# Optimization experiments

Measured on AMD Instinct MI355X. Metric: run time of the kernel, lower is better.

The kernel has to match this reference:

```python
import jax, jax.numpy as jnp
import numpy as np

N_NODES = 50000
N_EDGES = 800000
OBS_DIM = 25
HID = 128
EMB = 64
EDGE_DIM = 8
HEADS = 4
N_LAYERS = 3
COMM_RANGE = 1500.0
LN_EPS = 1e-5


def layernorm(x, g, b):
    mu = jnp.mean(x, axis=-1, keepdims=True)
    var = jnp.mean((x - mu) ** 2, axis=-1, keepdims=True)
    return (x - mu) / jnp.sqrt(var + LN_EPS) * g + b


def setup_inputs() -> dict:
    key = jax.random.key(0)
    ks = iter(jax.random.split(key, 64))

    def w(shape, s=0.05):
        return (jax.random.normal(next(ks), shape, jnp.float32) * s).astype(jnp.float32)

    inp = {}
    inp["observations"] = jax.random.normal(next(ks), (N_NODES, OBS_DIM), jnp.float32)
    inp["positions"] = jax.random.uniform(next(ks), (N_NODES, 2), jnp.float32) * 1000.0
    inp["edge_index"] = jax.random.randint(next(ks), (2, N_EDGES), 0, N_NODES, jnp.int32)
    # node encoder (obs_encoder branch: Linear-LN-ReLU-Linear-ReLU)
    inp["enc_w1"] = w((OBS_DIM, HID)); inp["enc_b1"] = w((HID,), 0.01)
    inp["enc_ln_g"] = jnp.ones((HID,), jnp.float32); inp["enc_ln_b"] = jnp.zeros((HID,), jnp.float32)
    inp["enc_w2"] = w((HID, EMB)); inp["enc_b2"] = w((EMB,), 0.01)
    cat_dim = 2 * EMB + EDGE_DIM  # 136
    # per-layer GNN params, stacked over layers
    inp["msg_w1"] = w((N_LAYERS, cat_dim, HID)); inp["msg_b1"] = w((N_LAYERS, HID), 0.01)
    inp["msg_w2"] = w((N_LAYERS, HID, EMB)); inp["msg_b2"] = w((N_LAYERS, EMB), 0.01)
    inp["att_w1"] = w((N_LAYERS, cat_dim, HID)); inp["att_b1"] = w((N_LAYERS, HID), 0.01)
    inp["att_w2"] = w((N_LAYERS, HID, HEADS)); inp["att_b2"] = w((N_LAYERS, HEADS), 0.01)
    inp["upd_w1"] = w((N_LAYERS, 2 * EMB, HID)); inp["upd_b1"] = w((N_LAYERS, HID), 0.01)
    inp["upd_w2"] = w((N_LAYERS, HID, EMB)); inp["upd_b2"] = w((N_LAYERS, EMB), 0.01)
    inp["ln_g"] = jnp.ones((N_LAYERS, EMB), jnp.float32); inp["ln_b"] = jnp.zeros((N_LAYERS, EMB), jnp.float32)
    # output projection
    inp["out_w1"] = w((EMB, HID)); inp["out_b1"] = w((HID,), 0.01)
    inp["out_w2"] = w((HID, EMB)); inp["out_b2"] = w((EMB,), 0.01)
    return inp


def reference(observations, positions, edge_index,
              enc_w1, enc_b1, enc_ln_g, enc_ln_b, enc_w2, enc_b2,
              msg_w1, msg_b1, msg_w2, msg_b2,
              att_w1, att_b1, att_w2, att_b2,
              upd_w1, upd_b1, upd_w2, upd_b2,
              ln_g, ln_b,
              out_w1, out_b1, out_w2, out_b2):
    n = observations.shape[0]
    # --- node encoder (use_full_obs=True path) ---
    h = observations @ enc_w1 + enc_b1
    h = jax.nn.relu(layernorm(h, enc_ln_g, enc_ln_b))
    x = jax.nn.relu(h @ enc_w2 + enc_b2)  # [N, EMB]

    # --- edge features (build_graph math, edges given) ---
    src, dst = edge_index[0], edge_index[1]
    rel = positions[dst] - positions[src]                    # [E, 2]
    dist = jnp.linalg.norm(rel, axis=-1, keepdims=True)      # [E, 1]
    rel_n = rel / (dist + 1e-6)
    dist_n = dist / COMM_RANGE
    angle = jnp.arctan2(rel[:, 1], rel[:, 0])[:, None]
    edge_attr = jnp.concatenate(
        [dist_n, rel_n, jnp.cos(angle), jnp.sin(angle), dist_n ** 2,
         jnp.zeros((rel.shape[0], 2), x.dtype)], axis=-1)    # [E, 8]

    # --- GNN communication layers (PyG: x_i = target = dst, x_j = source = src,
    #     aggregate to dst; dropout inactive at inference) ---
    for l in range(N_LAYERS):
        cat = jnp.concatenate([x[dst], x[src], edge_attr], axis=-1)       # [E, 136]
        m = jax.nn.relu(cat @ msg_w1[l] + msg_b1[l]) @ msg_w2[l] + msg_b2[l]   # [E, EMB]
        a = jax.nn.relu(cat @ att_w1[l] + att_b1[l]) @ att_w2[l] + att_b2[l]   # [E, HEADS]
        wgt = jnp.mean(jax.nn.softmax(a, axis=-1), axis=-1, keepdims=True)     # [E, 1]
        aggr = jax.ops.segment_sum(m * wgt, dst, num_segments=n)               # [N, EMB]
        upd_in = jnp.concatenate([x, aggr], axis=-1)                            # [N, 2*EMB]
        upd = jax.nn.relu(upd_in @ upd_w1[l] + upd_b1[l]) @ upd_w2[l] + upd_b2[l]
        x = layernorm(x + upd, ln_g[l], ln_b[l])

    # --- output projection ---
    return jax.nn.relu(x @ out_w1 + out_b1) @ out_w2 + out_b2
```

## Files before the change

### kernel.cpp

```cpp
#include <hip/hip_runtime.h>
#include <hip/hip_bf16.h>

typedef unsigned short ushort_t;
typedef unsigned int uint_t;

constexpr int OBS  = 25;
constexpr int HID  = 128;
constexpr int EMB  = 64;
constexpr int CAT  = 136;
constexpr int NN   = 50000;

constexpr int TE      = 128;
constexpr int ETHR    = 256;
constexpr int K1PAD   = 148;
constexpr int K2PAD   = 140;
constexpr int K1STEPS = 9;
constexpr int K2STEPS = 8;

constexpr int TB = 128;

typedef __attribute__((ext_vector_type(8)))  short bf16x8;
typedef __attribute__((ext_vector_type(16))) float f32x16;
typedef __attribute__((ext_vector_type(4)))  uint_t uint4v;

__device__ __forceinline__ ushort_t f2bf(float f) {
    union { float f; uint_t u; } v; v.f = f;
    uint_t r = v.u + 0x7FFFu + ((v.u >> 16) & 1u);
    return (ushort_t)(r >> 16);
}

__device__ __forceinline__ bf16x8 ld8(const ushort_t* p) {
    uint2 lo = *reinterpret_cast<const uint2*>(p);
    uint2 hi = *reinterpret_cast<const uint2*>(p + 4);
    uint4 u = make_uint4(lo.x, lo.y, hi.x, hi.y);
    return __builtin_bit_cast(bf16x8, u);
}

#define CROW(R, LHI) (4 * (LHI) + ((R) & 3) + 8 * ((R) >> 2))

__global__ __launch_bounds__(256) void k_hist(
    const int* __restrict__ dst, int* __restrict__ hist, int ne)
{
    int e = blockIdx.x * 256 + threadIdx.x;
    if (e < ne) atomicAdd(&hist[dst[e]], 1);
}

__global__ __launch_bounds__(512) void k_scan1(
    const int* __restrict__ hist, int* __restrict__ scanned,
    int* __restrict__ bsum, int nk)
{
    __shared__ int s[512];
    int t = threadIdx.x, i = blockIdx.x * 512 + t;
    int v = (i < nk) ? hist[i] : 0;
    s[t] = v; __syncthreads();
#pragma unroll
    for (int off = 1; off < 512; off <<= 1) {
        int x = (t >= off) ? s[t - off] : 0;
        __syncthreads();
        s[t] += x;
        __syncthreads();
    }
    if (i < nk) scanned[i] = s[t] - v;
    if (t == 511) bsum[blockIdx.x] = s[511];
}

__global__ __launch_bounds__(512) void k_scan3(
    int* __restrict__ scanned, const int* __restrict__ bsum, int nk)
{
    __shared__ int pref;
    if (threadIdx.x == 0) {
        int run = 0;
        for (int b = 0; b < (int)blockIdx.x; ++b) run += bsum[b];
        pref = run;
    }
    __syncthreads();
    int i = blockIdx.x * 512 + threadIdx.x;
    if (i < nk) scanned[i] += pref;
}

__global__ __launch_bounds__(256) void k_scatter_feat(
    const float* __restrict__ pos, const int* __restrict__ src,
    const int* __restrict__ dst, int* __restrict__ ofs,
    uint4v* __restrict__ eab4, int ne)
{
    int e = blockIdx.x * 256 + threadIdx.x;
    if (e >= ne) return;
    int s = src[e], d = dst[e];
    float rx = pos[d * 2 + 0] - pos[s * 2 + 0];
    float ry = pos[d * 2 + 1] - pos[s * 2 + 1];
    float dist = sqrtf(rx * rx + ry * ry);
    float inv = 1.f / (dist + 1e-6f);
    float dn = dist * (1.f / 1500.f);
    uint_t ux = (uint_t)f2bf(dn) | ((uint_t)f2bf(rx * inv) << 16);
    uint_t uy = (uint_t)f2bf(ry * inv) | ((dist > 0.f ? 0u : 1u) << 16);
    int p = atomicAdd(&ofs[d], 1);
    uint4v ev = { ux, uy, (uint_t)s, (uint_t)d };
    eab4[p] = ev;
}

__global__ __launch_bounds__(256) void k_prep(
    const float* __restrict__ w1, const float* __restrict__ w2,
    ushort_t* __restrict__ w1t, ushort_t* __restrict__ w2t)
{
    int t = blockIdx.x * 256 + threadIdx.x;
    const int n1 = 3 * HID * K1PAD;
    if (t < n1) {
        int l = t / (HID * K1PAD), rem = t % (HID * K1PAD);
        int c = rem / K1PAD, k = rem % K1PAD;
        float v = (k < CAT) ? w1[(size_t)l * CAT * HID + (size_t)k * HID + c] : 0.f;
        w1t[t] = f2bf(v);
    }
    const int n2 = 3 * EMB * K2PAD;
    if (t < n2) {
        int l = t / (EMB * K2PAD), rem = t % (EMB * K2PAD);
        int c = rem / K2PAD, k = rem % K2PAD;
        float v = (k < HID) ? w2[(size_t)l * HID * EMB + (size_t)k * EMB + c] : 0.f;
        w2t[t] = f2bf(v);
    }
}

constexpr int EKP = 36;
__global__ __launch_bounds__(256, 1) void k_encoder_mfma(
    const float* __restrict__ obs,
    const float* __restrict__ w1, const float* __restrict__ b1,
    const float* __restrict__ lng, const float* __restrict__ lnb,
    const float* __restrict__ w2, const float* __restrict__ b2,
    float* __restrict__ x, ushort_t* __restrict__ xb, int n)
{
    __shared__ __align__(16) ushort_t s_OB[TB * EKP];
    __shared__ __align__(16) ushort_t s_B1[HID * EKP];
    __shared__ __align__(16) float    s_G[TB * 132];
    __shared__ __align__(16) ushort_t s_H[TB * K2PAD];
    __shared__ __align__(16) ushort_t s_W2[EMB * K2PAD];

    const int tid = threadIdx.x;
    const int lane = tid & 63, wid = tid >> 6;
    const int wr = wid >> 1, wc = wid & 1;
    const int l31 = lane & 31, lhi = lane >> 5;
    const int n0 = blockIdx.x * TB;

    for (int i = tid; i < TB * 32; i += 256) {
        int row = i >> 5, k = i & 31;
        int gn = n0 + row;
        float v = (gn < n && k < OBS) ? obs[(size_t)gn * OBS + k] : 0.f;
        s_OB[row * EKP + k] = f2bf(v);
    }
    for (int i = tid; i < 32 * HID; i += 256) {
        int k = i >> 7, c = i & 127;
        float v = (k < OBS) ? w1[k * HID + c] : 0.f;
        s_B1[c * EKP + k] = f2bf(v);
    }
    __syncthreads();

    f32x16 a00, a01, a10, a11;
    {
        float bv0 = b1[wc * 64 + l31], bv1 = b1[wc * 64 + 32 + l31];
#pragma unroll
        for (int i = 0; i < 16; ++i) { a00[i] = bv0; a01[i] = bv1; a10[i] = bv0; a11[i] = bv1; }
    }
    {
        const ushort_t* aR0 = s_OB + (wr * 64 + l31) * EKP;
        const ushort_t* aR1 = aR0 + 32 * EKP;
        const ushort_t* bR0 = s_B1 + (wc * 64 + l31) * EKP;
        const ushort_t* bR1 = bR0 + 32 * EKP;
        const int koff = lhi * 8;
#pragma unroll
        for (int s = 0; s < 2; ++s) {
            const int ke = s * 16 + koff;
            bf16x8 av0 = ld8(aR0 + ke), av1 = ld8(aR1 + ke);
            bf16x8 bv0 = ld8(bR0 + ke), bv1 = ld8(bR1 + ke);
            a00 = __builtin_amdgcn_mfma_f32_32x32x16_bf16(av0, bv0, a00, 0, 0, 0);
            a01 = __builtin_amdgcn_mfma_f32_32x32x16_bf16(av0, bv1, a01, 0, 0, 0);
            a10 = __builtin_amdgcn_mfma_f32_32x32x16_bf16(av1, bv0, a10, 0, 0, 0);
            a11 = __builtin_amdgcn_mfma_f32_32x32x16_bf16(av1, bv1, a11, 0, 0, 0);
        }
    }
#define WRITE_G(ACC, SUB, NC)                                                  \
    {                                                                          \
        const int col = wc * 64 + (NC) * 32 + l31;                             \
        _Pragma("unroll")                                                      \
        for (int r = 0; r < 16; ++r) {                                         \
            int row = wr * 64 + (SUB) * 32 + CROW(r, lhi);                     \
            s_G[row * 132 + col] = ACC[r];                                     \
        }                                                                      \
    }
    WRITE_G(a00, 0, 0) WRITE_G(a01, 0, 1) WRITE_G(a10, 1, 0) WRITE_G(a11, 1, 1)
#undef WRITE_G
    __syncthreads();

    for (int i = tid; i < HID * EMB; i += 256) {
        int k = i >> 6, c = i & 63;
        s_W2[c * K2PAD + k] = f2bf(w2[i]);
    }
    if (tid < TB) {
        float sum = 0.f, sum2 = 0.f;
        const float* gr = s_G + tid * 132;
#pragma unroll 8
        for (int q = 0; q < HID; ++q) { float v = gr[q]; sum += v; sum2 += v * v; }
        float mu = sum * (1.f / HID);
        float var = fmaxf(sum2 * (1.f / HID) - mu * mu, 0.f);
        float rs = 1.f / sqrtf(var + 1e-5f);
        ushort_t* hr = s_H + tid * K2PAD;
#pragma unroll 8
        for (int q = 0; q < HID; ++q) {
            float v = (gr[q] - mu) * rs * lng[q] + lnb[q];
            hr[q] = f2bf(fmaxf(v, 0.f));
        }
    }
    __syncthreads();

    f32x16 c0, c1;
    {
        float bv = b2[wc * 32 + l31];
#pragma unroll
        for (int i = 0; i < 16; ++i) { c0[i] = bv; c1[i] = bv; }
    }
    {
        const ushort_t* aR0 = s_H + (wr * 64 + l31) * K2PAD;
        const ushort_t* aR1 = aR0 + 32 * K2PAD;
        const ushort_t* bR = s_W2 + (wc * 32 + l31) * K2PAD;
        const int koff = lhi * 8;
#pragma unroll
        for (int s = 0; s < K2STEPS; ++s) {
            const int ke = s * 16 + koff;
            bf16x8 av0 = ld8(aR0 + ke), av1 = ld8(aR1 + ke);
            bf16x8 bv = ld8(bR + ke);
            c0 = __builtin_amdgcn_mfma_f32_32x32x16_bf16(av0, bv, c0, 0, 0, 0);
            c1 = __builtin_amdgcn_mfma_f32_32x32x16_bf16(av1, bv, c1, 0, 0, 0);
        }
    }
    {
        const int col = wc * 32 + l31;
#define STORE_X(CC, SUB)                                                       \
        {                                                                      \
            _Pragma("unroll")                                                  \
            for (int r = 0; r < 16; ++r) {                                     \
                int row = wr * 64 + (SUB) * 32 + CROW(r, lhi);                 \
                int gn = n0 + row;                                             \
                if (gn < n) {                                                  \
                    float v = fmaxf(CC[r], 0.f);                               \
                    x[(size_t)gn * EMB + col] = v;                             \
                    xb[(size_t)gn * EMB + col] = f2bf(v);                      \
                }                                                              \
            }                                                                  \
        }
        STORE_X(c0, 0) STORE_X(c1, 1)
#undef STORE_X
    }
}

__global__ __launch_bounds__(ETHR, 4) void k_edge_mfma(
    const ushort_t* __restrict__ xb,
    const uint4v* __restrict__ eab4,
    const ushort_t* __restrict__ w1t,
    const float* __restrict__ b1,
    const ushort_t* __restrict__ w2t,
    const float* __restrict__ b2,
    float* __restrict__ aggr, int ne)
{
    __shared__ __align__(16) ushort_t s_A[TE * K1PAD];
    __shared__ int s_dst[TE];
    ushort_t* s_H = s_A;
    float*    s_M = reinterpret_cast<float*>(s_A);

    const int tid  = threadIdx.x;
    const int lane = tid & 63, wid = tid >> 6;
    const int wr = wid >> 1, wc = wid & 1;
    const int l31 = lane & 31, lhi = lane >> 5;
    const int e0 = blockIdx.x * TE;

    {
        const int e = tid >> 1, h = tid & 1, ge = e0 + e;
        ushort_t* arow = s_A + e * K1PAD;
        uint4v ev = eab4[ge];
        if (h == 0) {
            s_dst[e] = (int)ev.w;
            const uint2* sp = reinterpret_cast<const uint2*>(xb + (size_t)ev.w * EMB);
            uint2* dp = reinterpret_cast<uint2*>(arow);
#pragma unroll
            for (int i = 0; i < 16; ++i) dp[i] = sp[i];
        } else {
            const uint2* sp = reinterpret_cast<const uint2*>(xb + (size_t)ev.z * EMB);
            uint2* dp = reinterpret_cast<uint2*>(arow + EMB);
#pragma unroll
            for (int i = 0; i < 16; ++i) dp[i] = sp[i];
            uint_t dn_b = ev.x & 0xFFFFu, rxn_b = ev.x >> 16;
            uint_t ryn_b = ev.y & 0xFFFFu, flag = ev.y >> 16;
            uint_t cos_b = flag ? 0x3F80u : rxn_b;
            uint_t sin_b = flag ? 0u : ryn_b;
            union { uint_t u; float f; } cv; cv.u = dn_b << 16;
            uint_t dn2_b = (uint_t)f2bf(cv.f * cv.f);
            uint2* ap = reinterpret_cast<uint2*>(arow + 2 * EMB);
            ap[0] = make_uint2(dn_b | (rxn_b << 16), ryn_b | (cos_b << 16));
            ap[1] = make_uint2(sin_b | (dn2_b << 16), 0u);
            uint2* pp = reinterpret_cast<uint2*>(arow + CAT);
            pp[0] = make_uint2(0u, 0u); pp[1] = make_uint2(0u, 0u);
            pp[2] = make_uint2(0u, 0u);
        }
    }
    __syncthreads();

    f32x16 a00, a01, a10, a11;
    {
        float bv0 = b1[wc * 64 + l31], bv1 = b1[wc * 64 + 32 + l31];
#pragma unroll
        for (int i = 0; i < 16; ++i) { a00[i] = bv0; a01[i] = bv1; a10[i] = bv0; a11[i] = bv1; }
    }
    {
        const ushort_t* aR0 = s_A + (wr * 64 + l31) * K1PAD;
        const ushort_t* aR1 = aR0 + 32 * K1PAD;
        const ushort_t* bR0 = w1t + (wc * 64 + l31) * K1PAD;
        const ushort_t* bR1 = bR0 + 32 * K1PAD;
        const int koff = lhi * 8;
#pragma unroll
        for (int s = 0; s < K1STEPS; ++s) {
            const int ke = s * 16 + koff;
            bf16x8 av0 = ld8(aR0 + ke);
            bf16x8 av1 = ld8(aR1 + ke);
            bf16x8 bv0 = ld8(bR0 + ke);
            bf16x8 bv1 = ld8(bR1 + ke);
            a00 = __builtin_amdgcn_mfma_f32_32x32x16_bf16(av0, bv0, a00, 0, 0, 0);
            a01 = __builtin_amdgcn_mfma_f32_32x32x16_bf16(av0, bv1, a01, 0, 0, 0);
            a10 = __builtin_amdgcn_mfma_f32_32x32x16_bf16(av1, bv0, a10, 0, 0, 0);
            a11 = __builtin_amdgcn_mfma_f32_32x32x16_bf16(av1, bv1, a11, 0, 0, 0);
        }
    }
    __syncthreads();

#define WRITE_H(ACC, SUB, NC)                                                  \
    {                                                                          \
        const int col = wc * 64 + (NC) * 32 + l31;                             \
        _Pragma("unroll")                                                      \
        for (int r = 0; r < 16; ++r) {                                         \
            int row = wr * 64 + (SUB) * 32 + CROW(r, lhi);                     \
            s_H[row * K2PAD + col] = f2bf(fmaxf(ACC[r], 0.f));                 \
        }                                                                      \
    }
    WRITE_H(a00, 0, 0) WRITE_H(a01, 0, 1) WRITE_H(a10, 1, 0) WRITE_H(a11, 1, 1)
#undef WRITE_H
    __syncthreads();

    f32x16 c0, c1;
    {
        float bv = b2[wc * 32 + l31];
#pragma unroll
        for (int i = 0; i < 16; ++i) { c0[i] = bv; c1[i] = bv; }
    }
    {
        const ushort_t* aR0 = s_H + (wr * 64 + l31) * K2PAD;
        const ushort_t* aR1 = aR0 + 32 * K2PAD;
        const ushort_t* bR = w2t + (wc * 32 + l31) * K2PAD;
        const int koff = lhi * 8;
#pragma unroll
        for (int s = 0; s < K2STEPS; ++s) {
            const int ke = s * 16 + koff;
            bf16x8 av0 = ld8(aR0 + ke);
            bf16x8 av1 = ld8(aR1 + ke);
            bf16x8 bv = ld8(bR + ke);
            c0 = __builtin_amdgcn_mfma_f32_32x32x16_bf16(av0, bv, c0, 0, 0, 0);
            c1 = __builtin_amdgcn_mfma_f32_32x32x16_bf16(av1, bv, c1, 0, 0, 0);
        }
    }
    __syncthreads();

    {
        const int col = wc * 32 + l31;
#pragma unroll
        for (int r = 0; r < 16; ++r) {
            int row = wr * 64 + CROW(r, lhi);
            s_M[row * 68 + col] = c0[r] * 0.25f;
            s_M[(row + 32) * 68 + col] = c1[r] * 0.25f;
        }
    }
    __syncthreads();

    {
        const int col = tid & 63, g = tid >> 6, base = g * 32;
        int cur = s_dst[base];
        float acc = 0.f;
#pragma unroll 8
        for (int r = 0; r < 32; ++r) {
            int d = s_dst[base + r];
            float v = s_M[(base + r) * 68 + col];
            if (d != cur) {
                atomicAdd(aggr + (size_t)cur * EMB + col, acc);
                acc = 0.f; cur = d;
            }
            acc += v;
        }
        atomicAdd(aggr + (size_t)cur * EMB + col, acc);
    }
}

__global__ __launch_bounds__(256, 2) void k_update_mfma(
    float* __restrict__ x, ushort_t* __restrict__ xb,
    float* __restrict__ aggr,
    const float* __restrict__ w1, const float* __restrict__ b1,
    const float* __restrict__ w2, const float* __restrict__ b2,
    const float* __restrict__ g, const float* __restrict__ bb, int n)
{
    __shared__ __align__(16) ushort_t s_A[TB * K2PAD];
    __shared__ __align__(16) ushort_t s_B[TB * K2PAD];
    ushort_t* s_H  = s_A;
    ushort_t* s_W2 = s_B;
    float*    s_U  = reinterpret_cast<float*>(s_B);

    const int tid = threadIdx.x;
    const int lane = tid & 63, wid = tid >> 6;
    const int wr = wid >> 1, wc = wid & 1;
    const int l31 = lane & 31, lhi = lane >> 5;
    const int n0 = blockIdx.x * TB;

    {
        const int row = tid >> 1, h = tid & 1;
        const int gn = n0 + row;
        ushort_t* arow = s_A + row * K2PAD;
        if (h == 0) {
            uint2* dp = reinterpret_cast<uint2*>(arow);
            if (gn < n) {
                const uint2* sp = reinterpret_cast<const uint2*>(xb + (size_t)gn * EMB);
#pragma unroll
                for (int i = 0; i < 16; ++i) dp[i] = sp[i];
            } else {
                const uint2 z = make_uint2(0u, 0u);
#pragma unroll
                for (int i = 0; i < 16; ++i) dp[i] = z;
            }
        } else {
            if (gn < n) {
                float4* sp = reinterpret_cast<float4*>(aggr + (size_t)gn * EMB);
                const float4 z4 = make_float4(0.f, 0.f, 0.f, 0.f);
#pragma unroll
                for (int i = 0; i < 16; ++i) {
                    float4 v = sp[i];
                    sp[i] = z4;
                    ushort_t* qq = arow + EMB + i * 4;
                    qq[0] = f2bf(v.x); qq[1] = f2bf(v.y); qq[2] = f2bf(v.z); qq[3] = f2bf(v.w);
                }
            } else {
#pragma unroll
                for (int i = 0; i < 16; ++i) {
                    ushort_t* qq = arow + EMB + i * 4;
                    qq[0] = 0; qq[1] = 0; qq[2] = 0; qq[3] = 0;
                }
            }
        }
    }
    for (int i = tid; i < 128 * 128; i += 256) {
        int k = i >> 7, c = i & 127;
        s_B[c * K2PAD + k] = f2bf(w1[i]);
    }
    __syncthreads();

    f32x16 a00, a01, a10, a11;
    {
        float bv0 = b1[wc * 64 + l31], bv1 = b1[wc * 64 + 32 + l31];
#pragma unroll
        for (int i = 0; i < 16; ++i) { a00[i] = bv0; a01[i] = bv1; a10[i] = bv0; a11[i] = bv1; }
    }
    {
        const ushort_t* aR0 = s_A + (wr * 64 + l31) * K2PAD;
        const ushort_t* aR1 = aR0 + 32 * K2PAD;
        const ushort_t* bR0 = s_B + (wc * 64 + l31) * K2PAD;
        const ushort_t* bR1 = bR0 + 32 * K2PAD;
        const int koff = lhi * 8;
#pragma unroll
        for (int s = 0; s < K2STEPS; ++s) {
            const int ke = s * 16 + koff;
            bf16x8 av0 = ld8(aR0 + ke), av1 = ld8(aR1 + ke);
            bf16x8 bv0 = ld8(bR0 + ke), bv1 = ld8(bR1 + ke);
            a00 = __builtin_amdgcn_mfma_f32_32x32x16_bf16(av0, bv0, a00, 0, 0, 0);
            a01 = __builtin_amdgcn_mfma_f32_32x32x16_bf16(av0, bv1, a01, 0, 0, 0);
            a10 = __builtin_amdgcn_mfma_f32_32x32x16_bf16(av1, bv0, a10, 0, 0, 0);
            a11 = __builtin_amdgcn_mfma_f32_32x32x16_bf16(av1, bv1, a11, 0, 0, 0);
        }
    }
    __syncthreads();

#define WRITE_H(ACC, SUB, NC)                                                  \
    {                                                                          \
        const int col = wc * 64 + (NC) * 32 + l31;                             \
        _Pragma("unroll")                                                      \
        for (int r = 0; r < 16; ++r) {                                         \
            int row = wr * 64 + (SUB) * 32 + CROW(r, lhi);                     \
            s_H[row * K2PAD + col] = f2bf(fmaxf(ACC[r], 0.f));                 \
        }                                                                      \
    }
    WRITE_H(a00, 0, 0) WRITE_H(a01, 0, 1) WRITE_H(a10, 1, 0) WRITE_H(a11, 1, 1)
#undef WRITE_H
    for (int i = tid; i < HID * EMB; i += 256) {
        int k = i >> 6, c = i & 63;
        s_W2[c * K2PAD + k] = f2bf(w2[i]);
    }
    __syncthreads();

    f32x16 c0, c1;
    {
        float bv = b2[wc * 32 + l31];
#pragma unroll
        for (int i = 0; i < 16; ++i) { c0[i] = bv; c1[i] = bv; }
    }
    {
        const ushort_t* aR0 = s_H + (wr * 64 + l31) * K2PAD;
        const ushort_t* aR1 = aR0 + 32 * K2PAD;
        const ushort_t* bR = s_W2 + (wc * 32 + l31) * K2PAD;
        const int koff = lhi * 8;
#pragma unroll
        for (int s = 0; s < K2STEPS; ++s) {
            const int ke = s * 16 + koff;
            bf16x8 av0 = ld8(aR0 + ke), av1 = ld8(aR1 + ke);
            bf16x8 bv = ld8(bR + ke);
            c0 = __builtin_amdgcn_mfma_f32_32x32x16_bf16(av0, bv, c0, 0, 0, 0);
            c1 = __builtin_amdgcn_mfma_f32_32x32x16_bf16(av1, bv, c1, 0, 0, 0);
        }
    }
    __syncthreads();

    {
        const int col = wc * 32 + l31;
#pragma unroll
        for (int r = 0; r < 16; ++r) {
            int row = wr * 64 + CROW(r, lhi);
            s_U[row * 68 + col] = c0[r];
            s_U[(row + 32) * 68 + col] = c1[r];
        }
    }
    __syncthreads();

    if (tid < TB) {
        int gn = n0 + tid;
        if (gn < n) {
            const float* xr = x + (size_t)gn * EMB;
            float* ur = s_U + tid * 68;
            float sum = 0.f, sum2 = 0.f;
#pragma unroll 8
            for (int q = 0; q < EMB; ++q) {
                float v = xr[q] + ur[q];
                ur[q] = v;
                sum += v; sum2 += v * v;
            }
            float mu = sum * (1.f / EMB);
            float var = fmaxf(sum2 * (1.f / EMB) - mu * mu, 0.f);
            float rs = 1.f / sqrtf(var + 1e-5f);
            float* xo = x + (size_t)gn * EMB;
            ushort_t* xbo = xb + (size_t)gn * EMB;
#pragma unroll 8
            for (int q = 0; q < EMB; ++q) {
                float v = (ur[q] - mu) * rs * g[q] + bb[q];
                xo[q] = v;
                xbo[q] = f2bf(v);
            }
        }
    }
}

constexpr int OKP = 68;
__global__ __launch_bounds__(256, 2) void k_output_mfma(
    const ushort_t* __restrict__ xb,
    const float* __restrict__ w1, const float* __restrict__ b1,
    const float* __restrict__ w2, const float* __restrict__ b2,
    float* __restrict__ out, int n)
{
    __shared__ __align__(16) ushort_t s_A[TB * OKP];
    __shared__ __align__(16) ushort_t s_B[HID * OKP];
    __shared__ __align__(16) ushort_t s_H[TB * K2PAD];
    __shared__ __align__(16) ushort_t s_W2[EMB * K2PAD];

    const int tid = threadIdx.x;
    const int lane = tid & 63, wid = tid >> 6;
    const int wr = wid >> 1, wc = wid & 1;
    const int l31 = lane & 31, lhi = lane >> 5;
    const int n0 = blockIdx.x * TB;

    for (int i = tid; i < TB * 16; i += 256) {
        int row = i >> 4, q = i & 15;
        int gn = n0 + row;
        uint2 v = make_uint2(0u, 0u);
        if (gn < n) v = reinterpret_cast<const uint2*>(xb + (size_t)gn * EMB)[q];
        *reinterpret_cast<uint2*>(s_A + row * OKP + q * 4) = v;
    }
    for (int i = tid; i < EMB * HID; i += 256) {
        int k = i >> 7, c = i & 127;
        s_B[c * OKP + k] = f2bf(w1[i]);
    }
    for (int i = tid; i < HID * EMB; i += 256) {
        int k = i >> 6, c = i & 63;
        s_W2[c * K2PAD + k] = f2bf(w2[i]);
    }
    __syncthreads();

    f32x16 a00, a01, a10, a11;
    {
        float bv0 = b1[wc * 64 + l31], bv1 = b1[wc * 64 + 32 + l31];
#pragma unroll
        for (int i = 0; i < 16; ++i) { a00[i] = bv0; a01[i] = bv1; a10[i] = bv0; a11[i] = bv1; }
    }
    {
        const ushort_t* aR0 = s_A + (wr * 64 + l31) * OKP;
        const ushort_t* aR1 = aR0 + 32 * OKP;
        const ushort_t* bR0 = s_B + (wc * 64 + l31) * OKP;
        const ushort_t* bR1 = bR0 + 32 * OKP;
        const int koff = lhi * 8;
#pragma unroll
        for (int s = 0; s < 4; ++s) {
            const int ke = s * 16 + koff;
            bf16x8 av0 = ld8(aR0 + ke), av1 = ld8(aR1 + ke);
            bf16x8 bv0 = ld8(bR0 + ke), bv1 = ld8(bR1 + ke);
            a00 = __builtin_amdgcn_mfma_f32_32x32x16_bf16(av0, bv0, a00, 0, 0, 0);
            a01 = __builtin_amdgcn_mfma_f32_32x32x16_bf16(av0, bv1, a01, 0, 0, 0);
            a10 = __builtin_amdgcn_mfma_f32_32x32x16_bf16(av1, bv0, a10, 0, 0, 0);
            a11 = __builtin_amdgcn_mfma_f32_32x32x16_bf16(av1, bv1, a11, 0, 0, 0);
        }
    }
    __syncthreads();

#define WRITE_H(ACC, SUB, NC)                                                  \
    {                                                                          \
        const int col = wc * 64 + (NC) * 32 + l31;                             \
        _Pragma("unroll")                                                      \
        for (int r = 0; r < 16; ++r) {                                         \
            int row = wr * 64 + (SUB) * 32 + CROW(r, lhi);                     \
            s_H[row * K2PAD + col] = f2bf(fmaxf(ACC[r], 0.f));                 \
        }                                                                      \
    }
    WRITE_H(a00, 0, 0) WRITE_H(a01, 0, 1) WRITE_H(a10, 1, 0) WRITE_H(a11, 1, 1)
#undef WRITE_H
    __syncthreads();

    f32x16 c0, c1;
    {
        float bv = b2[wc * 32 + l31];
#pragma unroll
        for (int i = 0; i < 16; ++i) { c0[i] = bv; c1[i] = bv; }
    }
    {
        const ushort_t* aR0 = s_H + (wr * 64 + l31) * K2PAD;
        const ushort_t* aR1 = aR0 + 32 * K2PAD;
        const ushort_t* bR = s_W2 + (wc * 32 + l31) * K2PAD;
        const int koff = lhi * 8;
#pragma unroll
        for (int s = 0; s < K2STEPS; ++s) {
            const int ke = s * 16 + koff;
            bf16x8 av0 = ld8(aR0 + ke), av1 = ld8(aR1 + ke);
            bf16x8 bv = ld8(bR + ke);
            c0 = __builtin_amdgcn_mfma_f32_32x32x16_bf16(av0, bv, c0, 0, 0, 0);
            c1 = __builtin_amdgcn_mfma_f32_32x32x16_bf16(av1, bv, c1, 0, 0, 0);
        }
    }
    {
        const int col = wc * 32 + l31;
#pragma unroll
        for (int r = 0; r < 16; ++r) {
            int row0 = wr * 64 + CROW(r, lhi);
            int g0 = n0 + row0, g1 = g0 + 32;
            if (g0 < n) out[(size_t)g0 * EMB + col] = c0[r];
            if (g1 < n) out[(size_t)g1 * EMB + col] = c1[r];
        }
    }
}

extern "C" void kernel_launch(void* const* d_in, const int* in_sizes, int n_in,
                              void* d_out, int out_size, void* d_ws, size_t ws_size,
                              hipStream_t stream)
{
    const float* obs     = (const float*)d_in[0];
    const float* pos     = (const float*)d_in[1];
    const int*   eidx    = (const int*)d_in[2];
    const float* enc_w1  = (const float*)d_in[3];
    const float* enc_b1  = (const float*)d_in[4];
    const float* enc_lng = (const float*)d_in[5];
    const float* enc_lnb = (const float*)d_in[6];
    const float* enc_w2  = (const float*)d_in[7];
    const float* enc_b2  = (const float*)d_in[8];
    const float* msg_w1  = (const float*)d_in[9];
    const float* msg_b1  = (const float*)d_in[10];
    const float* msg_w2  = (const float*)d_in[11];
    const float* msg_b2  = (const float*)d_in[12];
    const float* upd_w1  = (const float*)d_in[17];
    const float* upd_b1  = (const float*)d_in[18];
    const float* upd_w2  = (const float*)d_in[19];
    const float* upd_b2  = (const float*)d_in[20];
    const float* ln_g    = (const float*)d_in[21];
    const float* ln_b    = (const float*)d_in[22];
    const float* out_w1  = (const float*)d_in[23];
    const float* out_b1  = (const float*)d_in[24];
    const float* out_w2  = (const float*)d_in[25];
    const float* out_b2  = (const float*)d_in[26];

    const int n  = in_sizes[0] / OBS;
    const int ne = in_sizes[2] / 2;
    const int* src = eidx;
    const int* dst = eidx + ne;

    char* ws = (char*)d_ws;
    float*    x     = (float*)ws;
    ushort_t* xbuf  = (ushort_t*)(ws + 12800000);
    uint4v*   eab4  = (uint4v*)(ws + 19200000);
    float*    aggr  = (float*)(ws + 32000000);
    ushort_t* w1t   = (ushort_t*)(ws + 44800000);
    ushort_t* w2t   = (ushort_t*)(ws + 44913664);
    int*      hist  = (int*)(ws + 44967424);
    int*      scan  = (int*)(ws + 45167424);
    int*      bsum  = (int*)(ws + 45367424);

    const int NB1 = (NN + 511) / 512;
    const int nb  = (n + TB - 1) / TB;

    hipMemsetAsync(hist, 0, NN * sizeof(int), stream);
    k_hist<<<(ne + 255) / 256, 256, 0, stream>>>(dst, hist, ne);
    k_scan1<<<NB1, 512, 0, stream>>>(hist, scan, bsum, NN);
    k_scan3<<<NB1, 512, 0, stream>>>(scan, bsum, NN);
    k_scatter_feat<<<(ne + 255) / 256, 256, 0, stream>>>(pos, src, dst, scan,
                                                         eab4, ne);

    k_prep<<<(3 * HID * K1PAD + 255) / 256, 256, 0, stream>>>(msg_w1, msg_w2, w1t, w2t);
    k_encoder_mfma<<<nb, 256, 0, stream>>>(obs, enc_w1, enc_b1, enc_lng, enc_lnb,
                                           enc_w2, enc_b2, x, xbuf, n);
    hipMemsetAsync(aggr, 0, (size_t)n * EMB * sizeof(float), stream);

    for (int l = 0; l < 3; ++l) {
        k_edge_mfma<<<ne / TE, ETHR, 0, stream>>>(
            xbuf, eab4,
            w1t + (size_t)l * HID * K1PAD, msg_b1 + (size_t)l * HID,
            w2t + (size_t)l * EMB * K2PAD, msg_b2 + (size_t)l * EMB,
            aggr, ne);
        k_update_mfma<<<nb, 256, 0, stream>>>(
            x, xbuf, aggr,
            upd_w1 + (size_t)l * 2 * EMB * HID, upd_b1 + (size_t)l * HID,
            upd_w2 + (size_t)l * HID * EMB, upd_b2 + (size_t)l * EMB,
            ln_g + (size_t)l * EMB, ln_b + (size_t)l * EMB, n);
    }
    k_output_mfma<<<nb, 256, 0, stream>>>(
        xbuf, out_w1, out_b1, out_w2, out_b2, (float*)d_out, n);
}
```

Measured before the change: 754.9 us.

## Double edge-kernel threads to 512 and split MFMA tiles across eight waves

```diff
diff --git a/kernel.cpp b/kernel.cpp
--- a/kernel.cpp
+++ b/kernel.cpp
@@ -11,7 +11,7 @@
 constexpr int NN   = 50000;
 
 constexpr int TE      = 128;
-constexpr int ETHR    = 256;
+constexpr int ETHR    = 512;
 constexpr int K1PAD   = 148;
 constexpr int K2PAD   = 140;
 constexpr int K1STEPS = 9;
@@ -249,7 +249,7 @@
     }
 }
 
-__global__ __launch_bounds__(ETHR, 4) void k_edge_mfma(
+__global__ __launch_bounds__(ETHR, 8) void k_edge_mfma(
     const ushort_t* __restrict__ xb,
     const uint4v* __restrict__ eab4,
     const ushort_t* __restrict__ w1t,
@@ -270,7 +270,7 @@
     const int e0 = blockIdx.x * TE;
 
     {
-        const int e = tid >> 1, h = tid & 1, ge = e0 + e;
+        const int e = tid >> 2, h = tid & 3, ge = e0 + e;
         ushort_t* arow = s_A + e * K1PAD;
         uint4v ev = eab4[ge];
         if (h == 0) {
@@ -278,12 +278,22 @@
             const uint2* sp = reinterpret_cast<const uint2*>(xb + (size_t)ev.w * EMB);
             uint2* dp = reinterpret_cast<uint2*>(arow);
 #pragma unroll
-            for (int i = 0; i < 16; ++i) dp[i] = sp[i];
-        } else {
+            for (int i = 0; i < 8; ++i) dp[i] = sp[i];
+        } else if (h == 1) {
+            const uint2* sp = reinterpret_cast<const uint2*>(xb + (size_t)ev.w * EMB) + 8;
+            uint2* dp = reinterpret_cast<uint2*>(arow) + 8;
+#pragma unroll
+            for (int i = 0; i < 8; ++i) dp[i] = sp[i];
+        } else if (h == 2) {
             const uint2* sp = reinterpret_cast<const uint2*>(xb + (size_t)ev.z * EMB);
             uint2* dp = reinterpret_cast<uint2*>(arow + EMB);
 #pragma unroll
-            for (int i = 0; i < 16; ++i) dp[i] = sp[i];
+            for (int i = 0; i < 8; ++i) dp[i] = sp[i];
+        } else {
+            const uint2* sp = reinterpret_cast<const uint2*>(xb + (size_t)ev.z * EMB) + 8;
+            uint2* dp = reinterpret_cast<uint2*>(arow + EMB) + 8;
+#pragma unroll
+            for (int i = 0; i < 8; ++i) dp[i] = sp[i];
             uint_t dn_b = ev.x & 0xFFFFu, rxn_b = ev.x >> 16;
             uint_t ryn_b = ev.y & 0xFFFFu, flag = ev.y >> 16;
             uint_t cos_b = flag ? 0x3F80u : rxn_b;
@@ -300,65 +310,58 @@
     }
     __syncthreads();
 
-    f32x16 a00, a01, a10, a11;
+    f32x16 a0, a1;
     {
         float bv0 = b1[wc * 64 + l31], bv1 = b1[wc * 64 + 32 + l31];
 #pragma unroll
-        for (int i = 0; i < 16; ++i) { a00[i] = bv0; a01[i] = bv1; a10[i] = bv0; a11[i] = bv1; }
-    }
-    {
-        const ushort_t* aR0 = s_A + (wr * 64 + l31) * K1PAD;
-        const ushort_t* aR1 = aR0 + 32 * K1PAD;
+        for (int i = 0; i < 16; ++i) { a0[i] = bv0; a1[i] = bv1; }
+    }
+    {
+        const ushort_t* aR = s_A + (wr * 32 + l31) * K1PAD;
         const ushort_t* bR0 = w1t + (wc * 64 + l31) * K1PAD;
         const ushort_t* bR1 = bR0 + 32 * K1PAD;
         const int koff = lhi * 8;
 #pragma unroll
         for (int s = 0; s < K1STEPS; ++s) {
             const int ke = s * 16 + koff;
-            bf16x8 av0 = ld8(aR0 + ke);
-            bf16x8 av1 = ld8(aR1 + ke);
+            bf16x8 av = ld8(aR + ke);
             bf16x8 bv0 = ld8(bR0 + ke);
             bf16x8 bv1 = ld8(bR1 + ke);
-            a00 = __builtin_amdgcn_mfma_f32_32x32x16_bf16(av0, bv0, a00, 0, 0, 0);
-            a01 = __builtin_amdgcn_mfma_f32_32x32x16_bf16(av0, bv1, a01, 0, 0, 0);
-            a10 = __builtin_amdgcn_mfma_f32_32x32x16_bf16(av1, bv0, a10, 0, 0, 0);
-            a11 = __builtin_amdgcn_mfma_f32_32x32x16_bf16(av1, bv1, a11, 0, 0, 0);
-        }
-    }
-    __syncthreads();
-
-#define WRITE_H(ACC, SUB, NC)                                                  \
+            a0 = __builtin_amdgcn_mfma_f32_32x32x16_bf16(av, bv0, a0, 0, 0, 0);
+            a1 = __builtin_amdgcn_mfma_f32_32x32x16_bf16(av, bv1, a1, 0, 0, 0);
+        }
+    }
+    __syncthreads();
+
+#define WRITE_H(ACC, NC)                                                       \
     {                                                                          \
         const int col = wc * 64 + (NC) * 32 + l31;                             \
         _Pragma("unroll")                                                      \
         for (int r = 0; r < 16; ++r) {                                         \
-            int row = wr * 64 + (SUB) * 32 + CROW(r, lhi);                     \
+            int row = wr * 32 + CROW(r, lhi);                                  \
             s_H[row * K2PAD + col] = f2bf(fmaxf(ACC[r], 0.f));                 \
         }                                                                      \
     }
-    WRITE_H(a00, 0, 0) WRITE_H(a01, 0, 1) WRITE_H(a10, 1, 0) WRITE_H(a11, 1, 1)
+    WRITE_H(a0, 0) WRITE_H(a1, 1)
 #undef WRITE_H
     __syncthreads();
 
-    f32x16 c0, c1;
+    f32x16 c0;
     {
         float bv = b2[wc * 32 + l31];
 #pragma unroll
-        for (int i = 0; i < 16; ++i) { c0[i] = bv; c1[i] = bv; }
-    }
-    {
-        const ushort_t* aR0 = s_H + (wr * 64 + l31) * K2PAD;
-        const ushort_t* aR1 = aR0 + 32 * K2PAD;
+        for (int i = 0; i < 16; ++i) c0[i] = bv;
+    }
+    {
+        const ushort_t* aR = s_H + (wr * 32 + l31) * K2PAD;
         const ushort_t* bR = w2t + (wc * 32 + l31) * K2PAD;
         const int koff = lhi * 8;
 #pragma unroll
         for (int s = 0; s < K2STEPS; ++s) {
             const int ke = s * 16 + koff;
-            bf16x8 av0 = ld8(aR0 + ke);
-            bf16x8 av1 = ld8(aR1 + ke);
+            bf16x8 av = ld8(aR + ke);
             bf16x8 bv = ld8(bR + ke);
-            c0 = __builtin_amdgcn_mfma_f32_32x32x16_bf16(av0, bv, c0, 0, 0, 0);
-            c1 = __builtin_amdgcn_mfma_f32_32x32x16_bf16(av1, bv, c1, 0, 0, 0);
+            c0 = __builtin_amdgcn_mfma_f32_32x32x16_bf16(av, bv, c0, 0, 0, 0);
         }
     }
     __syncthreads();
@@ -367,14 +370,13 @@
         const int col = wc * 32 + l31;
 #pragma unroll
         for (int r = 0; r < 16; ++r) {
-            int row = wr * 64 + CROW(r, lhi);
+            int row = wr * 32 + CROW(r, lhi);
             s_M[row * 68 + col] = c0[r] * 0.25f;
-            s_M[(row + 32) * 68 + col] = c1[r] * 0.25f;
-        }
-    }
-    __syncthreads();
-
-    {
+        }
+    }
+    __syncthreads();
+
+    if (tid < 256) {
         const int col = tid & 63, g = tid >> 6, base = g * 32;
         int cur = s_dst[base];
         float acc = 0.f;
```

Result: faster. 713.8 us (-5.5%).
